# Optimization experiments

Measured on AMD Instinct MI355X. Metric: run time of the kernel, lower is better.

## Reference

```python
import jax, jax.numpy as jnp
import numpy as np

FILL = -1024.0


def setup_inputs() -> dict:
    key = jax.random.key(0)
    ks = jax.random.split(key, 8)
    B, Q, K, D, KD, VD = 4, 4096, 4096, 512, 64, 64
    s = 0.02  # small init scale for numeric sanity
    return {
        "x": jax.random.normal(ks[0], (B, Q, D), dtype=jnp.float32),
        "buffer": jax.random.normal(ks[1], (B, K, D), dtype=jnp.float32),
        "mask": jax.random.randint(ks[2], (B, Q, K), 0, 2) > 0,
        "Wq": jax.random.normal(ks[3], (KD, D), dtype=jnp.float32) * s,
        "bq": jnp.zeros((KD,), dtype=jnp.float32),
        "Wk": jax.random.normal(ks[4], (KD, D), dtype=jnp.float32) * s,
        "bk": jnp.zeros((KD,), dtype=jnp.float32),
        "Wv": jax.random.normal(ks[5], (VD, D), dtype=jnp.float32) * s,
        "bv": jnp.zeros((VD,), dtype=jnp.float32),
    }


def reference(x, buffer, mask, Wq, bq, Wk, bk, Wv, bv):
    key_dim = Wq.shape[0]
    query = x @ Wq.T + bq          # [B, Q, KD]
    keys = buffer @ Wk.T + bk      # [B, K, KD]
    vals = buffer @ Wv.T + bv      # [B, K, VD]
    logits = jnp.einsum('bqd,bkd->bqk', query, keys) / np.sqrt(key_dim).astype(np.float32)
    logits = jnp.where(mask, logits, FILL)
    # stable softmax (same math as exp(x - max) / sum)
    probs = jax.nn.softmax(logits, axis=-1)
    read = jnp.einsum('bqk,bkd->bqd', probs, vals)  # [B, Q, VD]
    return read
```

## Files before the change

### kernel.cpp

```cpp
#include <hip/hip_runtime.h>
#include <hip/hip_bf16.h>

typedef float f32x4 __attribute__((ext_vector_type(4)));
typedef __bf16 bf16x8 __attribute__((ext_vector_type(8)));
typedef unsigned long long u64;
typedef u64 u64x2 __attribute__((ext_vector_type(2)));

#define NB 4
#define NQ 4096
#define NK 4096
#define DIM 512
#define KD 64
#define PKW 128
#define NG64 (1 << 20)
#define PACK_BLOCKS 2048
#define PACK_WAVES (PACK_BLOCKS * 4)

__device__ inline bf16x8 load_cvt8(const float* __restrict__ p) {
    float4 f0 = *(const float4*)p;
    float4 f1 = *(const float4*)(p + 4);
    bf16x8 r;
    r[0] = (__bf16)f0.x; r[1] = (__bf16)f0.y; r[2] = (__bf16)f0.z; r[3] = (__bf16)f0.w;
    r[4] = (__bf16)f1.x; r[5] = (__bf16)f1.y; r[6] = (__bf16)f1.z; r[7] = (__bf16)f1.w;
    return r;
}

__global__ __launch_bounds__(256, 4) void prep_kernel(
        const float* __restrict__ x, const float* __restrict__ buf,
        const int* __restrict__ mask,
        const float* __restrict__ Wq, const float* __restrict__ bq,
        const float* __restrict__ Wk, const float* __restrict__ bk,
        const float* __restrict__ Wv, const float* __restrict__ bv,
        __bf16* __restrict__ Qb, __bf16* __restrict__ Kb, __bf16* __restrict__ Vt,
        unsigned* __restrict__ pk) {
    __shared__ __align__(16) float ps[4][32][66];

    const int tid = threadIdx.x;
    const int w = tid >> 6, l = tid & 63;

    if (blockIdx.x >= 1024) {
        const int wid = (blockIdx.x - 1024) * 4 + w;
        u64* pk64 = (u64*)pk;
        for (int g0 = wid * 4; g0 < NG64; g0 += PACK_WAVES * 4) {
            const int* mb = mask + (long)g0 * 64 + l;
            int m0 = mb[0];
            int m1 = mb[64];
            int m2 = mb[128];
            int m3 = mb[192];
            u64 b0 = __ballot(m0 != 0);
            u64 b1 = __ballot(m1 != 0);
            u64 b2 = __ballot(m2 != 0);
            u64 b3 = __ballot(m3 != 0);
            if (l == 0) {
                u64x2 v01 = {b0, b1}, v23 = {b2, b3};
                *(u64x2*)(pk64 + g0)     = v01;
                *(u64x2*)(pk64 + g0 + 2) = v23;
            }
        }
        return;
    }

    const int lr = l & 15, lk = l >> 4;
    const int rg = w >> 1, kh = w & 1;
    const bool is_q = blockIdx.x < 512;
    const int blk = is_q ? blockIdx.x : blockIdx.x - 512;
    const long rowbase = (long)blk * 32 + rg * 16;
    const int kbase = kh * 256;

    if (is_q) {
        f32x4 acc[4] = {};
        for (int kk = 0; kk < 256; kk += 32) {
            bf16x8 a = load_cvt8(x + (rowbase + lr) * DIM + kbase + kk + lk * 8);
#pragma unroll
            for (int nb = 0; nb < 4; nb++) {
                bf16x8 bw = load_cvt8(Wq + (long)(nb * 16 + lr) * DIM + kbase + kk + lk * 8);
                acc[nb] = __builtin_amdgcn_mfma_f32_16x16x32_bf16(a, bw, acc[nb], 0, 0, 0);
            }
        }
#pragma unroll
        for (int nb = 0; nb < 4; nb++)
#pragma unroll
            for (int i = 0; i < 4; i++)
                ps[kh * 2][rg * 16 + lk * 4 + i][nb * 16 + lr] = acc[nb][i];
        __syncthreads();
        for (int e = tid; e < 2048; e += 256) {
            int row = e >> 6, col = e & 63;
            float v = ps[0][row][col] + ps[2][row][col] + bq[col];
            Qb[((long)blk * 32 + row) * KD + col] = (__bf16)v;
        }
    } else {
        f32x4 acck[4] = {}, accv[4] = {};
        for (int kk = 0; kk < 256; kk += 32) {
            bf16x8 a = load_cvt8(buf + (rowbase + lr) * DIM + kbase + kk + lk * 8);
#pragma unroll
            for (int nb = 0; nb < 4; nb++) {
                bf16x8 bwk = load_cvt8(Wk + (long)(nb * 16 + lr) * DIM + kbase + kk + lk * 8);
                bf16x8 bwv = load_cvt8(Wv + (long)(nb * 16 + lr) * DIM + kbase + kk + lk * 8);
                acck[nb] = __builtin_amdgcn_mfma_f32_16x16x32_bf16(a, bwk, acck[nb], 0, 0, 0);
                accv[nb] = __builtin_amdgcn_mfma_f32_16x16x32_bf16(a, bwv, accv[nb], 0, 0, 0);
            }
        }
#pragma unroll
        for (int nb = 0; nb < 4; nb++)
#pragma unroll
            for (int i = 0; i < 4; i++) {
                ps[kh * 2 + 0][rg * 16 + lk * 4 + i][nb * 16 + lr] = acck[nb][i];
                ps[kh * 2 + 1][rg * 16 + lk * 4 + i][nb * 16 + lr] = accv[nb][i];
            }
        __syncthreads();
        for (int e = tid; e < 2048; e += 256) {
            int row = e >> 6, col = e & 63;
            float v = ps[0][row][col] + ps[2][row][col] + bk[col];
            Kb[((long)blk * 32 + row) * KD + col] = (__bf16)v;
        }
        for (int e = tid; e < 2048; e += 256) {
            int row = e & 31, col = e >> 5;
            float v = ps[1][row][col] + ps[3][row][col] + bv[col];
            long grow = (long)blk * 32 + row;
            int b = (int)(grow >> 12), kidx = (int)(grow & 4095);
            Vt[((long)b * KD + col) * NK + kidx] = (__bf16)v;
        }
    }
}

__global__ __launch_bounds__(512, 4) void attn_kernel(
        const __bf16* __restrict__ Qb, const __bf16* __restrict__ Kb,
        const __bf16* __restrict__ Vt, const unsigned* __restrict__ pk,
        float* __restrict__ out) {
    __shared__ __align__(16) char smem[36864];

    const int tid = threadIdx.x;
    const int w = tid >> 6, l = tid & 63;
    const int lr = l & 15, lk = l >> 4;
    const int b = blockIdx.x >> 8;
    const int q0 = (blockIdx.x & 255) * 16;
    const int k0 = w * 512;

    const __bf16* Qp = Qb + ((long)b * NQ + q0) * KD;
    const __bf16* Kp = Kb + (long)b * NK * KD;
    const __bf16* Vp = Vt + (long)b * KD * NK;
    const unsigned* mp = pk + ((long)b * NQ + q0) * PKW;

    __bf16 (*pl0)[72] = (__bf16(*)[72])(smem + w * 4608);
    __bf16 (*pl1)[72] = (__bf16(*)[72])(smem + w * 4608 + 2304);

    bf16x8 qa[2];
#pragma unroll
    for (int ks = 0; ks < 2; ks++)
        qa[ks] = *(const bf16x8*)(Qp + (long)lr * KD + ks * 32 + lk * 8);

    f32x4 o[4] = {};
    float l_i[4] = {0.f, 0.f, 0.f, 0.f};

    auto tile = [&](int kt, __bf16 (*pl)[72]) {
        f32x4 s[4] = {};
#pragma unroll
        for (int ks = 0; ks < 2; ks++)
#pragma unroll
            for (int nb = 0; nb < 4; nb++) {
                bf16x8 kb = *(const bf16x8*)(Kp + (long)(kt + nb * 16 + lr) * KD + ks * 32 + lk * 8);
                s[nb] = __builtin_amdgcn_mfma_f32_16x16x32_bf16(qa[ks], kb, s[nb], 0, 0, 0);
            }
        unsigned mw0[4], mw1[4];
#pragma unroll
        for (int i = 0; i < 4; i++) {
            uint2 mwv = *(const uint2*)(mp + (long)(lk * 4 + i) * PKW + (kt >> 5));
            mw0[i] = mwv.x; mw1[i] = mwv.y;
        }
#pragma unroll
        for (int nb = 0; nb < 4; nb++) {
            const unsigned bit = (unsigned)((nb * 16 + lr) & 31);
#pragma unroll
            for (int i = 0; i < 4; i++) {
                unsigned wv = (nb < 2) ? mw0[i] : mw1[i];
                float e = __expf(s[nb][i] * 0.125f);
                float p = ((wv >> bit) & 1u) ? e : 0.0f;
                __bf16 pb = (__bf16)p;
                pl[lk * 4 + i][nb * 16 + lr] = pb;
                l_i[i] += (float)pb;
            }
        }
#pragma unroll
        for (int ks = 0; ks < 2; ks++) {
            bf16x8 pa = *(const bf16x8*)&pl[lr][ks * 32 + lk * 8];
#pragma unroll
            for (int nb = 0; nb < 4; nb++) {
                bf16x8 vb = *(const bf16x8*)(Vp + (long)(nb * 16 + lr) * NK + kt + ks * 32 + lk * 8);
                o[nb] = __builtin_amdgcn_mfma_f32_16x16x32_bf16(pa, vb, o[nb], 0, 0, 0);
            }
        }
    };

#pragma unroll 1
    for (int kt = k0; kt < k0 + 512; kt += 128) {
        tile(kt, pl0);
        tile(kt + 64, pl1);
    }

#pragma unroll
    for (int i = 0; i < 4; i++) {
        float v = l_i[i];
        v += __shfl_xor(v, 1);
        v += __shfl_xor(v, 2);
        v += __shfl_xor(v, 4);
        v += __shfl_xor(v, 8);
        l_i[i] = v;
    }

    __syncthreads();
    float* o_s = (float*)smem;
    float* ml  = (float*)(smem + 8 * 16 * 66 * 4);
#pragma unroll
    for (int nb = 0; nb < 4; nb++)
#pragma unroll
        for (int i = 0; i < 4; i++)
            o_s[(w * 16 + lk * 4 + i) * 66 + nb * 16 + lr] = o[nb][i];
    if (lr == 0) {
#pragma unroll
        for (int i = 0; i < 4; i++)
            ml[w * 16 + lk * 4 + i] = l_i[i];
    }
    __syncthreads();
    for (int e = tid; e < 1024; e += 512) {
        int row = e >> 6, col = e & 63;
        float L = 0.f, O = 0.f;
#pragma unroll
        for (int ww = 0; ww < 8; ww++) {
            L += ml[ww * 16 + row];
            O += o_s[(ww * 16 + row) * 66 + col];
        }
        out[((long)b * NQ + q0 + row) * KD + col] = O / L;
    }
}

extern "C" void kernel_launch(void* const* d_in, const int* in_sizes, int n_in,
                              void* d_out, int out_size, void* d_ws, size_t ws_size,
                              hipStream_t stream) {
    const float* x      = (const float*)d_in[0];
    const float* buffer = (const float*)d_in[1];
    const int*   mask   = (const int*)d_in[2];
    const float* Wq     = (const float*)d_in[3];
    const float* bq     = (const float*)d_in[4];
    const float* Wk     = (const float*)d_in[5];
    const float* bk     = (const float*)d_in[6];
    const float* Wv     = (const float*)d_in[7];
    const float* bv     = (const float*)d_in[8];
    float* out = (float*)d_out;

    unsigned* pk = (unsigned*)d_ws;
    __bf16* Qb = (__bf16*)((char*)d_ws + (size_t)NB * NQ * PKW * 4);
    __bf16* Kb = Qb + (size_t)NB * NQ * KD;
    __bf16* Vt = Kb + (size_t)NB * NK * KD;

    prep_kernel<<<dim3(1024 + PACK_BLOCKS), dim3(256), 0, stream>>>(
        x, buffer, mask, Wq, bq, Wk, bk, Wv, bv, Qb, Kb, Vt, pk);
    attn_kernel<<<dim3(NB * (NQ / 16)), dim3(512), 0, stream>>>(Qb, Kb, Vt, pk, out);
}
```

Measured before the change: 226.1 us.

## Split mask packing into its own kernel, fold softmax scale into Q, remap blocks to XCDs

Mask bit-packing moves out of the fused prep kernel into a separate launch, and each wave now handles 8 ballots per iteration instead of 4. The 1/sqrt(d) scale is applied once when Q is written rather than per logit in the attention loop. Attention blocks are remapped so each XCD works on one batch half, which should improve L2 locality for K and V. Unroll pragmas are added to the projection loops; the extra kernel launch and the loss of overlap between packing and projection are the costs.

Result: slower. 264.1 us (+16.8%).

```diff
diff --git a/kernel.cpp b/kernel.cpp
--- a/kernel.cpp
+++ b/kernel.cpp
@@ -16,6 +16,31 @@
 #define PACK_BLOCKS 2048
 #define PACK_WAVES (PACK_BLOCKS * 4)
 
+__global__ __launch_bounds__(256, 8) void pack_kernel(
+        const int* __restrict__ mask, unsigned* __restrict__ pk) {
+    const int tid = threadIdx.x;
+    const int w = tid >> 6, l = tid & 63;
+    const int wid = blockIdx.x * 4 + w;
+    u64* pk64 = (u64*)pk;
+#pragma unroll 1
+    for (int g0 = wid * 8; g0 < NG64; g0 += PACK_WAVES * 8) {
+        const int* mb = mask + (long)g0 * 64 + l;
+        int m[8];
+#pragma unroll
+        for (int j = 0; j < 8; j++) m[j] = mb[j * 64];
+        u64 bb[8];
+#pragma unroll
+        for (int j = 0; j < 8; j++) bb[j] = __ballot(m[j] != 0);
+        if (l == 0) {
+#pragma unroll
+            for (int j = 0; j < 4; j++) {
+                u64x2 v = {bb[2 * j], bb[2 * j + 1]};
+                *(u64x2*)(pk64 + g0 + 2 * j) = v;
+            }
+        }
+    }
+}
+
 __device__ inline bf16x8 load_cvt8(const float* __restrict__ p) {
     float4 f0 = *(const float4*)p;
     float4 f1 = *(const float4*)(p + 4);
@@ -25,41 +50,16 @@
     return r;
 }
 
-__global__ __launch_bounds__(256, 4) void prep_kernel(
+__global__ __launch_bounds__(256, 4) void proj_kernel(
         const float* __restrict__ x, const float* __restrict__ buf,
-        const int* __restrict__ mask,
         const float* __restrict__ Wq, const float* __restrict__ bq,
         const float* __restrict__ Wk, const float* __restrict__ bk,
         const float* __restrict__ Wv, const float* __restrict__ bv,
-        __bf16* __restrict__ Qb, __bf16* __restrict__ Kb, __bf16* __restrict__ Vt,
-        unsigned* __restrict__ pk) {
+        __bf16* __restrict__ Qb, __bf16* __restrict__ Kb, __bf16* __restrict__ Vt) {
     __shared__ __align__(16) float ps[4][32][66];
 
     const int tid = threadIdx.x;
     const int w = tid >> 6, l = tid & 63;
-
-    if (blockIdx.x >= 1024) {
-        const int wid = (blockIdx.x - 1024) * 4 + w;
-        u64* pk64 = (u64*)pk;
-        for (int g0 = wid * 4; g0 < NG64; g0 += PACK_WAVES * 4) {
-            const int* mb = mask + (long)g0 * 64 + l;
-            int m0 = mb[0];
-            int m1 = mb[64];
-            int m2 = mb[128];
-            int m3 = mb[192];
-            u64 b0 = __ballot(m0 != 0);
-            u64 b1 = __ballot(m1 != 0);
-            u64 b2 = __ballot(m2 != 0);
-            u64 b3 = __ballot(m3 != 0);
-            if (l == 0) {
-                u64x2 v01 = {b0, b1}, v23 = {b2, b3};
-                *(u64x2*)(pk64 + g0)     = v01;
-                *(u64x2*)(pk64 + g0 + 2) = v23;
-            }
-        }
-        return;
-    }
-
     const int lr = l & 15, lk = l >> 4;
     const int rg = w >> 1, kh = w & 1;
     const bool is_q = blockIdx.x < 512;
@@ -69,6 +69,7 @@
 
     if (is_q) {
         f32x4 acc[4] = {};
+#pragma unroll 4
         for (int kk = 0; kk < 256; kk += 32) {
             bf16x8 a = load_cvt8(x + (rowbase + lr) * DIM + kbase + kk + lk * 8);
 #pragma unroll
@@ -85,11 +86,12 @@
         __syncthreads();
         for (int e = tid; e < 2048; e += 256) {
             int row = e >> 6, col = e & 63;
-            float v = ps[0][row][col] + ps[2][row][col] + bq[col];
+            float v = (ps[0][row][col] + ps[2][row][col] + bq[col]) * 0.125f;
             Qb[((long)blk * 32 + row) * KD + col] = (__bf16)v;
         }
     } else {
         f32x4 acck[4] = {}, accv[4] = {};
+#pragma unroll 2
         for (int kk = 0; kk < 256; kk += 32) {
             bf16x8 a = load_cvt8(buf + (rowbase + lr) * DIM + kbase + kk + lk * 8);
 #pragma unroll
@@ -132,8 +134,10 @@
     const int tid = threadIdx.x;
     const int w = tid >> 6, l = tid & 63;
     const int lr = l & 15, lk = l >> 4;
-    const int b = blockIdx.x >> 8;
-    const int q0 = (blockIdx.x & 255) * 16;
+    const int orig = blockIdx.x;
+    const int xcd = orig & 7, slot = orig >> 3;
+    const int b = xcd >> 1;
+    const int q0 = ((xcd & 1) * 128 + slot) * 16;
     const int k0 = w * 512;
 
     const __bf16* Qp = Qb + ((long)b * NQ + q0) * KD;
@@ -173,7 +177,7 @@
 #pragma unroll
             for (int i = 0; i < 4; i++) {
                 unsigned wv = (nb < 2) ? mw0[i] : mw1[i];
-                float e = __expf(s[nb][i] * 0.125f);
+                float e = __expf(s[nb][i]);
                 float p = ((wv >> bit) & 1u) ? e : 0.0f;
                 __bf16 pb = (__bf16)p;
                 pl[lk * 4 + i][nb * 16 + lr] = pb;
@@ -252,7 +256,7 @@
     __bf16* Kb = Qb + (size_t)NB * NQ * KD;
     __bf16* Vt = Kb + (size_t)NB * NK * KD;
 
-    prep_kernel<<<dim3(1024 + PACK_BLOCKS), dim3(256), 0, stream>>>(
-        x, buffer, mask, Wq, bq, Wk, bk, Wv, bv, Qb, Kb, Vt, pk);
+    pack_kernel<<<dim3(PACK_BLOCKS), dim3(256), 0, stream>>>(mask, pk);
+    proj_kernel<<<dim3(1024), dim3(256), 0, stream>>>(x, buffer, Wq, bq, Wk, bk, Wv, bv, Qb, Kb, Vt);
     attn_kernel<<<dim3(NB * (NQ / 16)), dim3(512), 0, stream>>>(Qb, Kb, Vt, pk, out);
 }
```
